# Optimization experiments

Measured on AMD Instinct MI355X. Metric: run time of the kernel, lower is better.

## Reference

```python
import jax, jax.numpy as jnp
import numpy as np

N_NODES = 50000
W_IN = 256
W_OUT = 256
HEADS = 8
D_HEAD = W_OUT // HEADS
NUM_EDGE = 3
N_EDGES = 800000
NEG_SLOPE = 0.2


def setup_inputs() -> dict:
    key = jax.random.key(0)
    ks = jax.random.split(key, 10)
    x = jax.random.normal(ks[0], (N_NODES, W_IN), dtype=jnp.float32)
    adj = jax.random.randint(ks[1], (NUM_EDGE, 2, N_EDGES), 0, N_NODES, dtype=jnp.int64)
    sw = 1.0 / np.sqrt(W_IN)
    # Per-edge-type GATConv params, stacked on leading edge-type axis
    Ws = jax.random.normal(ks[2], (NUM_EDGE, W_IN, HEADS * D_HEAD), dtype=jnp.float32) * sw
    a_l = jax.random.normal(ks[3], (NUM_EDGE, HEADS, D_HEAD), dtype=jnp.float32) * 0.1
    a_r = jax.random.normal(ks[4], (NUM_EDGE, HEADS, D_HEAD), dtype=jnp.float32) * 0.1
    bias = jnp.zeros((NUM_EDGE, HEADS * D_HEAD), dtype=jnp.float32)
    # Semantic attention layer: Linear(w_out -> 1)
    att_w = jax.random.normal(ks[5], (W_OUT, 1), dtype=jnp.float32) * (1.0 / np.sqrt(W_OUT))
    att_b = jnp.zeros((1,), dtype=jnp.float32)
    return {"x": x, "adj": adj, "Ws": Ws, "a_l": a_l, "a_r": a_r,
            "bias": bias, "att_w": att_w, "att_b": att_b}


def _gat(x, edge_index, W, al, ar, b):
    # x: [N, W_IN]; edge_index: [2, E]; W: [W_IN, H*D]; al/ar: [H, D]; b: [H*D]
    N = x.shape[0]
    h = (x @ W).reshape(N, HEADS, D_HEAD)            # [N, H, D]
    src, dst = edge_index[0], edge_index[1]
    el = jnp.einsum('nhd,hd->nh', h, al)             # src-side scores [N, H]
    er = jnp.einsum('nhd,hd->nh', h, ar)             # dst-side scores [N, H]
    e = jax.nn.leaky_relu(el[src] + er[dst], NEG_SLOPE)   # [E, H]
    # segment softmax over incoming edges of each dst node
    m = jax.ops.segment_max(e, dst, num_segments=N)       # [N, H]
    e = jnp.exp(e - m[dst])
    s = jax.ops.segment_sum(e, dst, num_segments=N)       # [N, H]
    alpha = e / (s[dst] + 1e-9)                           # [E, H]
    out = jax.ops.segment_sum(alpha[:, :, None] * h[src], dst, num_segments=N)
    return out.reshape(N, HEADS * D_HEAD) + b             # concat heads [N, W_OUT]


def reference(x, adj, Ws, a_l, a_r, bias, att_w, att_b):
    outs = [_gat(x, adj[i], Ws[i], a_l[i], a_r[i], bias[i]) for i in range(NUM_EDGE)]
    stacked = jnp.stack(outs, axis=1)                     # [N, T, W_OUT]
    # AttentionLayer: scores = Linear(stacked) viewed as [N, 1, T]; NO softmax (faithful)
    att = (stacked @ att_w + att_b).reshape(-1, 1, NUM_EDGE)  # [N, 1, T]
    return jnp.matmul(att, stacked).squeeze(1)            # [N, W_OUT]
```

## Files before the change

kernel.cpp:

```cpp
#include <hip/hip_runtime.h>

#define N_NODES 50000
#define W_IN    256
#define W_OUT   256
#define HEADS   8
#define NUM_T   3
#define N_EDGES 800000
#define NEG_SLOPE 0.2f

#define NB      128
#define BSH     9
#define BNODES  512
#define P1_EPT  16
#define P1_CHUNK (256 * P1_EPT)
#define P1_BLOCKS ((N_EDGES + P1_CHUNK - 1) / P1_CHUNK)
#define NB_USED ((N_NODES + BNODES - 1) / BNODES)

#define GEMM_BLOCKS ((N_NODES + 63) / 64)
#define GATHER_BLOCKS ((N_NODES + 3) / 4)
#define GEMM_SMEM 29696

typedef __attribute__((ext_vector_type(8))) short bf16x8;
typedef __attribute__((ext_vector_type(4))) float f32x4;

__device__ __forceinline__ unsigned short f2b(float f) {
    unsigned u = __float_as_uint(f);
    u = (u + 0x7fffu + ((u >> 16) & 1u)) >> 16;
    return (unsigned short)u;
}
__device__ __forceinline__ float blo(unsigned u) { return __uint_as_float(u << 16); }
__device__ __forceinline__ float bhi(unsigned u) { return __uint_as_float(u & 0xffff0000u); }

__global__ __launch_bounds__(256) void convert_x(const float* __restrict__ x,
                                                 unsigned short* __restrict__ xb) {
    const size_t i = ((size_t)blockIdx.x * 256 + threadIdx.x) * 4;
    const float4 v = *(const float4*)(x + i);
    ushort4 o;
    o.x = f2b(v.x); o.y = f2b(v.y); o.z = f2b(v.z); o.w = f2b(v.w);
    *(ushort4*)(xb + i) = o;
}

__global__ __launch_bounds__(256) void convert_W(const float* __restrict__ Wsrc,
                                                 unsigned short* __restrict__ Wt) {
    const int t = blockIdx.y;
    const int gid = blockIdx.x * 256 + threadIdx.x;
    const int k = gid >> 8, n = gid & 255;
    Wt[(size_t)t * 65536 + (size_t)n * 256 + k] = f2b(Wsrc[(size_t)t * 65536 + gid]);
}

__global__ __launch_bounds__(256) void p1_hist(const int* __restrict__ adj,
                                               int* __restrict__ bucket_cnt) {
    __shared__ int lh[NB];
    const int t = blockIdx.y;
    const int tid = threadIdx.x;
    if (tid < NB) lh[tid] = 0;
    __syncthreads();

    const int* dstp = adj + (size_t)t * 2 * N_EDGES + N_EDGES;
    const int e0 = blockIdx.x * P1_CHUNK + tid * P1_EPT;
#pragma unroll
    for (int i = 0; i < P1_EPT; ++i) {
        const int e = e0 + i;
        if (e < N_EDGES) atomicAdd(&lh[dstp[e] >> BSH], 1);
    }
    __syncthreads();
    if (tid < NB && lh[tid] > 0) atomicAdd(&bucket_cnt[t * NB + tid], lh[tid]);
}

__global__ __launch_bounds__(128) void p1_scan(const int* __restrict__ bucket_cnt,
                                               int* __restrict__ bucket_ptr,
                                               int* __restrict__ bucket_cur) {
    __shared__ int s[NB];
    const int tid = threadIdx.x;
    for (int t = 0; t < NUM_T; ++t) {
        const int v = bucket_cnt[t * NB + tid];
        s[tid] = v;
        __syncthreads();
        for (int off = 1; off < NB; off <<= 1) {
            int o = (tid >= off) ? s[tid - off] : 0;
            __syncthreads();
            s[tid] += o;
            __syncthreads();
        }
        const int incl = s[tid];
        const int excl = incl - v;
        bucket_ptr[t * (NB + 1) + tid] = excl;
        bucket_cur[t * NB + tid] = excl;
        if (tid == NB - 1) bucket_ptr[t * (NB + 1) + NB] = incl;
        __syncthreads();
    }
}

__global__ __launch_bounds__(256) void p1_scatter(const int* __restrict__ adj,
                                                  int* __restrict__ bucket_cur,
                                                  uint2* __restrict__ part) {
    __shared__ int lh[NB];
    __shared__ int loff[NB];
    __shared__ int lbase[NB];
    __shared__ uint2 buf[P1_CHUNK];
    const int t = blockIdx.y;
    const int tid = threadIdx.x;
    const int lane = tid & 63;
    const int wave = tid >> 6;
    if (tid < NB) lh[tid] = 0;
    __syncthreads();

    const int* srcp = adj + (size_t)t * 2 * N_EDGES;
    const int* dstp = srcp + N_EDGES;
    const int e0 = blockIdx.x * P1_CHUNK + tid * P1_EPT;

    int es[P1_EPT], ed[P1_EPT], rk[P1_EPT];
#pragma unroll
    for (int i = 0; i < P1_EPT; ++i) {
        const int e = e0 + i;
        if (e < N_EDGES) {
            es[i] = srcp[e];
            ed[i] = dstp[e];
            rk[i] = atomicAdd(&lh[ed[i] >> BSH], 1);
        } else {
            ed[i] = -1;
        }
    }
    __syncthreads();

    if (tid < NB && lh[tid] > 0)
        lbase[tid] = atomicAdd(&bucket_cur[t * NB + tid], lh[tid]);
    if (wave == 0) {
        const int c0 = lh[lane * 2], c1 = lh[lane * 2 + 1];
        const int s = c0 + c1;
        int run = s;
        for (int off = 1; off < 64; off <<= 1) {
            const int o = __shfl_up(run, off);
            if (lane >= off) run += o;
        }
        const int base = run - s;
        loff[lane * 2] = base;
        loff[lane * 2 + 1] = base + c0;
    }
    __syncthreads();

#pragma unroll
    for (int i = 0; i < P1_EPT; ++i)
        if (ed[i] >= 0)
            buf[loff[ed[i] >> BSH] + rk[i]] =
                make_uint2((unsigned)es[i], (unsigned)ed[i]);
    __syncthreads();

    uint2* pt = part + (size_t)t * N_EDGES;
    int nvalid = N_EDGES - blockIdx.x * P1_CHUNK;
    if (nvalid > P1_CHUNK) nvalid = P1_CHUNK;
    for (int idx = tid; idx < nvalid; idx += 256) {
        const uint2 e = buf[idx];
        const int b = (int)(e.y >> BSH);
        pt[lbase[b] + (idx - loff[b])] = e;
    }
}

__global__ __launch_bounds__(256) void p2_csr(const uint2* __restrict__ part,
                                              const int* __restrict__ bucket_ptr,
                                              int* __restrict__ row_ptr_all,
                                              int* __restrict__ csr_all) {
    __shared__ int sc[BNODES];
    const int b = blockIdx.x;
    const int t = blockIdx.y;
    const int tid = threadIdx.x;
    const int lane = tid & 63;
    const int wave = tid >> 6;

    const uint2* pt = part + (size_t)t * N_EDGES;
    int* row_ptr = row_ptr_all + (size_t)t * (N_NODES + 1);
    int* csr = csr_all + (size_t)t * N_EDGES;

    const int bp0 = bucket_ptr[t * (NB + 1) + b];
    const int bp1 = bucket_ptr[t * (NB + 1) + b + 1];
    const int node0 = b * BNODES;
    int nn = N_NODES - node0; if (nn > BNODES) nn = BNODES;

    sc[tid] = 0; sc[tid + 256] = 0;
    __syncthreads();

    for (int idx = bp0 + tid; idx < bp1; idx += 256)
        atomicAdd(&sc[pt[idx].y - node0], 1);
    __syncthreads();

    if (wave == 0) {
        int v[8], ex[8];
        int s = 0;
#pragma unroll
        for (int i = 0; i < 8; ++i) { v[i] = sc[lane * 8 + i]; ex[i] = s; s += v[i]; }
        int run = s;
        for (int off = 1; off < 64; off <<= 1) {
            int o = __shfl_up(run, off);
            if (lane >= off) run += o;
        }
        const int base = run - s;
#pragma unroll
        for (int i = 0; i < 8; ++i) sc[lane * 8 + i] = base + ex[i];
    }
    __syncthreads();

    for (int i = tid; i < nn; i += 256) row_ptr[node0 + i] = bp0 + sc[i];
    if (b == NB_USED - 1 && tid == 0) row_ptr[N_NODES] = N_EDGES;
    __syncthreads();

    for (int idx = bp0 + tid; idx < bp1; idx += 256) {
        const uint2 e = pt[idx];
        const int pos = bp0 + atomicAdd(&sc[e.y - node0], 1);
        csr[pos] = (int)e.x;
    }
}

__device__ __forceinline__ void gemm_body(const int bm, const int tid,
                                          unsigned char* smem,
                                          const unsigned short* __restrict__ xb,
                                          const unsigned short* __restrict__ Wt,
                                          const float* __restrict__ al,
                                          const float* __restrict__ ar,
                                          unsigned short* __restrict__ H,
                                          float* __restrict__ el,
                                          float* __restrict__ er) {
    unsigned short* As = (unsigned short*)smem;
    unsigned short* Bs = (unsigned short*)(smem + 5120);
    float* els = (float*)(smem + 25600);
    float* ers = (float*)(smem + 27648);

    const int wave = tid >> 6;
    const int lane = tid & 63;
    const int quad = lane >> 4;
    const int l16 = lane & 15;
    const int m0 = bm * 64;

    f32x4 acc[4][4] = {};

    const int arow = tid >> 2;
    const int achunk = (tid & 3) * 8;
    int gm = m0 + arow;
    if (gm > N_NODES - 1) gm = N_NODES - 1;
    const unsigned short* aptr = xb + (size_t)gm * W_IN + achunk;

    for (int k0 = 0; k0 < W_IN; k0 += 32) {
        const uint4 av = *(const uint4*)(aptr + k0);
        *(uint4*)&As[arow * 40 + achunk] = av;
#pragma unroll
        for (int i = 0; i < 4; ++i) {
            const int idx = i * 256 + tid;
            const int brow = idx >> 2;
            const int bch = (idx & 3) * 8;
            const uint4 bv = *(const uint4*)(Wt + (size_t)brow * W_IN + k0 + bch);
            *(uint4*)&Bs[brow * 40 + bch] = bv;
        }
        __syncthreads();

        bf16x8 af[4], bfr[4];
#pragma unroll
        for (int mi = 0; mi < 4; ++mi)
            af[mi] = *(const bf16x8*)&As[(mi * 16 + l16) * 40 + quad * 8];
#pragma unroll
        for (int ni = 0; ni < 4; ++ni)
            bfr[ni] = *(const bf16x8*)&Bs[(wave * 64 + ni * 16 + l16) * 40 + quad * 8];
#pragma unroll
        for (int mi = 0; mi < 4; ++mi)
#pragma unroll
            for (int ni = 0; ni < 4; ++ni)
                acc[mi][ni] = __builtin_amdgcn_mfma_f32_16x16x32_bf16(
                    af[mi], bfr[ni], acc[mi][ni], 0, 0, 0);
        __syncthreads();
    }

#pragma unroll
    for (int mi = 0; mi < 4; ++mi)
#pragma unroll
        for (int reg = 0; reg < 4; ++reg) {
            const int gr = m0 + mi * 16 + quad * 4 + reg;
            if (gr < N_NODES)
#pragma unroll
                for (int ni = 0; ni < 4; ++ni)
                    H[(size_t)gr * W_OUT + wave * 64 + ni * 16 + l16] =
                        f2b(acc[mi][ni][reg]);
        }

    float al4[4], ar4[4];
#pragma unroll
    for (int ni = 0; ni < 4; ++ni) {
        const int c = wave * 64 + ni * 16 + l16;
        al4[ni] = al[c];
        ar4[ni] = ar[c];
    }
#pragma unroll
    for (int mi = 0; mi < 4; ++mi) {
        float pl[4][2] = {}, pr[4][2] = {};
#pragma unroll
        for (int ni = 0; ni < 4; ++ni) {
            const int hl = ni >> 1;
#pragma unroll
            for (int reg = 0; reg < 4; ++reg) {
                pl[reg][hl] += acc[mi][ni][reg] * al4[ni];
                pr[reg][hl] += acc[mi][ni][reg] * ar4[ni];
            }
        }
#pragma unroll
        for (int off = 1; off < 16; off <<= 1)
#pragma unroll
            for (int reg = 0; reg < 4; ++reg)
#pragma unroll
                for (int hl = 0; hl < 2; ++hl) {
                    pl[reg][hl] += __shfl_xor(pl[reg][hl], off);
                    pr[reg][hl] += __shfl_xor(pr[reg][hl], off);
                }
        if (l16 == 0)
#pragma unroll
            for (int reg = 0; reg < 4; ++reg)
#pragma unroll
                for (int hl = 0; hl < 2; ++hl) {
                    const int row = mi * 16 + quad * 4 + reg;
                    els[row * 8 + wave * 2 + hl] = pl[reg][hl];
                    ers[row * 8 + wave * 2 + hl] = pr[reg][hl];
                }
    }
    __syncthreads();

    int nn = N_NODES - m0; if (nn > 64) nn = 64;
    const int nn8 = nn * 8;
    const int i = tid * 4;
    if (i < nn8) {
        *(float4*)(el + (size_t)m0 * 8 + i) = *(float4*)&els[i];
        *(float4*)(er + (size_t)m0 * 8 + i) = *(float4*)&ers[i];
    }
}

__device__ __forceinline__ void gather_body(const int node, const int lane,
                                            const int* __restrict__ csr_src,
                                            const int* __restrict__ row_ptr,
                                            const float* __restrict__ el,
                                            const float* __restrict__ er,
                                            const unsigned short* __restrict__ H,
                                            unsigned short* __restrict__ ot) {
    const int half = lane >> 5;
    const int d8 = lane & 31;
    const int hh = d8 >> 2;

    const int beg = row_ptr[node];
    const int deg = row_ptr[node + 1] - beg;
    const float erv = er[(size_t)node * HEADS + hh];

    float2 acc[4] = {};
    float ssum = 0.f;

    if (deg > 0) {
        int mysrc = (lane < deg) ? csr_src[beg + lane] : 0;
        const int npairs = (deg + 1) >> 1;

        int src0 = __shfl(mysrc, half);
        uint4 u0 = *(const uint4*)(H + (size_t)src0 * W_OUT + d8 * 8);
        float elv0 = el[(size_t)src0 * HEADS + hh];

        for (int q = 0; q < npairs; ++q) {
            int src1 = 0; uint4 u1 = u0; float elv1 = 0.f;
            const int q1 = q + 1;
            if (q1 < npairs) {
                if ((q1 & 31) == 0) {
                    const int cb = beg + (q1 >> 5) * 64;
                    mysrc = (cb + lane < beg + deg) ? csr_src[cb + lane] : 0;
                }
                src1 = __shfl(mysrc, (2 * q1 + half) & 63);
                u1 = *(const uint4*)(H + (size_t)src1 * W_OUT + d8 * 8);
                elv1 = el[(size_t)src1 * HEADS + hh];
            }
            float v = elv0 + erv;
            v = (v > 0.f) ? v : NEG_SLOPE * v;
            const float w = (2 * q + half < deg) ? __expf(v) : 0.f;
            acc[0].x += w * blo(u0.x); acc[0].y += w * bhi(u0.x);
            acc[1].x += w * blo(u0.y); acc[1].y += w * bhi(u0.y);
            acc[2].x += w * blo(u0.z); acc[2].y += w * bhi(u0.z);
            acc[3].x += w * blo(u0.w); acc[3].y += w * bhi(u0.w);
            ssum += w;
            src0 = src1; u0 = u1; elv0 = elv1;
        }
    }

#pragma unroll
    for (int i = 0; i < 4; ++i) {
        acc[i].x += __shfl_xor(acc[i].x, 32);
        acc[i].y += __shfl_xor(acc[i].y, 32);
    }
    ssum += __shfl_xor(ssum, 32);

    if (half == 0) {
        const float inv = 1.f / (ssum + 1e-9f);
        unsigned short o8[8];
#pragma unroll
        for (int i = 0; i < 4; ++i) {
            o8[2 * i]     = f2b(acc[i].x * inv);
            o8[2 * i + 1] = f2b(acc[i].y * inv);
        }
        *(uint4*)(ot + (size_t)node * W_OUT + d8 * 8) = *(const uint4*)o8;
    }
}

__global__ __launch_bounds__(256) void gemm_fused(const unsigned short* __restrict__ xb,
                                                  const unsigned short* __restrict__ Wt,
                                                  const float* __restrict__ al,
                                                  const float* __restrict__ ar,
                                                  unsigned short* __restrict__ H,
                                                  float* __restrict__ el,
                                                  float* __restrict__ er) {
    __shared__ __attribute__((aligned(16))) unsigned char smem[GEMM_SMEM];
    const size_t t = blockIdx.y;
    gemm_body(blockIdx.x, threadIdx.x, smem, xb,
              Wt + t * 65536, al + t * 256, ar + t * 256,
              H + t * (size_t)N_NODES * W_OUT,
              el + t * (size_t)N_NODES * HEADS,
              er + t * (size_t)N_NODES * HEADS);
}

__global__ __launch_bounds__(256) void gat_gather(const int* __restrict__ csr_src,
                                                  const int* __restrict__ row_ptr,
                                                  const float* __restrict__ el,
                                                  const float* __restrict__ er,
                                                  const unsigned short* __restrict__ H,
                                                  unsigned short* __restrict__ ot) {
    const int node = (blockIdx.x * blockDim.x + threadIdx.x) >> 6;
    if (node >= N_NODES) return;
    const size_t t = blockIdx.y;
    gather_body(node, threadIdx.x & 63,
                csr_src + t * N_EDGES, row_ptr + t * (N_NODES + 1),
                el + t * (size_t)N_NODES * HEADS,
                er + t * (size_t)N_NODES * HEADS,
                H + t * (size_t)N_NODES * W_OUT,
                ot + t * (size_t)N_NODES * W_OUT);
}

__global__ __launch_bounds__(256) void combine(const unsigned short* __restrict__ ot,
                                               const float* __restrict__ bias,
                                               const float* __restrict__ att_w,
                                               const float* __restrict__ att_b,
                                               float* __restrict__ out) {
    const int gw = (blockIdx.x * blockDim.x + threadIdx.x) >> 6;
    const int lane = threadIdx.x & 63;
    if (gw >= N_NODES) return;

    const float4 aw = *(const float4*)(att_w + lane * 4);
    const size_t base = (size_t)gw * W_OUT + lane * 4;
    const size_t tstride = (size_t)N_NODES * W_OUT;

    float4 v[NUM_T];
    float p[NUM_T];
#pragma unroll
    for (int t = 0; t < NUM_T; ++t) {
        const uint2 u = *(const uint2*)(ot + t * tstride + base);
        const float4 bv = *(const float4*)(bias + t * W_OUT + lane * 4);
        float4 hv;
        hv.x = blo(u.x) + bv.x;
        hv.y = bhi(u.x) + bv.y;
        hv.z = blo(u.y) + bv.z;
        hv.w = bhi(u.y) + bv.w;
        v[t] = hv;
        p[t] = hv.x * aw.x + hv.y * aw.y + hv.z * aw.z + hv.w * aw.w;
    }
#pragma unroll
    for (int off = 1; off < 64; off <<= 1) {
        p[0] += __shfl_xor(p[0], off);
        p[1] += __shfl_xor(p[1], off);
        p[2] += __shfl_xor(p[2], off);
    }
    const float ab = att_b[0];
    const float a0 = p[0] + ab, a1 = p[1] + ab, a2 = p[2] + ab;
    float4 o;
    o.x = a0 * v[0].x + a1 * v[1].x + a2 * v[2].x;
    o.y = a0 * v[0].y + a1 * v[1].y + a2 * v[2].y;
    o.z = a0 * v[0].z + a1 * v[1].z + a2 * v[2].z;
    o.w = a0 * v[0].w + a1 * v[1].w + a2 * v[2].w;
    *(float4*)(out + base) = o;
}

extern "C" void kernel_launch(void* const* d_in, const int* in_sizes, int n_in,
                              void* d_out, int out_size, void* d_ws, size_t ws_size,
                              hipStream_t stream) {
    const float* x     = (const float*)d_in[0];
    const int*   adj   = (const int*)d_in[1];
    const float* Ws    = (const float*)d_in[2];
    const float* a_l   = (const float*)d_in[3];
    const float* a_r   = (const float*)d_in[4];
    const float* bias  = (const float*)d_in[5];
    const float* att_w = (const float*)d_in[6];
    const float* att_b = (const float*)d_in[7];
    float* out = (float*)d_out;

    const size_t XB_B  = (size_t)N_NODES * W_IN * 2;
    const size_t H_B   = (size_t)N_NODES * W_OUT * 2;
    const size_t WT_B  = (size_t)NUM_T * 65536 * 2;
    const size_t EL_B  = (size_t)N_NODES * HEADS * 4;
    const size_t CSR_B = (size_t)NUM_T * N_EDGES * 4;
    const size_t RP_B  = (size_t)NUM_T * (N_NODES + 1) * 4;
    const size_t MISC_B = (size_t)NUM_T * (NB * 2 + NB + 1) * 4 + 4096;

    const size_t need_merged = XB_B + NUM_T * H_B + WT_B + NUM_T * H_B
                             + 2 * NUM_T * EL_B + CSR_B + RP_B + MISC_B;
    const bool merged = (ws_size >= need_merged);

    char* w = (char*)d_ws;
    unsigned short* xb = (unsigned short*)w; w += XB_B;
    unsigned short* H  = (unsigned short*)w; w += merged ? NUM_T * H_B : H_B;
    unsigned short* Wt = (unsigned short*)w; w += WT_B;
    unsigned short* ot = (unsigned short*)w; w += NUM_T * H_B;
    float* el = (float*)w; w += merged ? NUM_T * EL_B : EL_B;
    float* er = (float*)w; w += merged ? NUM_T * EL_B : EL_B;
    int* csr_src = (int*)w; w += CSR_B;
    int* row_ptr = (int*)w; w += RP_B;
    int* bucket_cnt = (int*)w; w += NUM_T * NB * 4;
    int* bucket_ptr = (int*)w; w += NUM_T * (NB + 1) * 4;
    int* bucket_cur = (int*)w; w += NUM_T * NB * 4;
    uint2* part = (uint2*)ot;

    hipMemsetAsync(bucket_cnt, 0, NUM_T * NB * sizeof(int), stream);
    convert_x<<<12500, 256, 0, stream>>>(x, xb);
    convert_W<<<dim3(256, NUM_T), 256, 0, stream>>>(Ws, Wt);
    p1_hist<<<dim3(P1_BLOCKS, NUM_T), 256, 0, stream>>>(adj, bucket_cnt);
    p1_scan<<<1, 128, 0, stream>>>(bucket_cnt, bucket_ptr, bucket_cur);
    p1_scatter<<<dim3(P1_BLOCKS, NUM_T), 256, 0, stream>>>(adj, bucket_cur, part);
    p2_csr<<<dim3(NB_USED, NUM_T), 256, 0, stream>>>(part, bucket_ptr, row_ptr,
                                                     csr_src);

    if (merged) {
        gemm_fused<<<dim3(GEMM_BLOCKS, NUM_T), 256, 0, stream>>>(
            xb, Wt, a_l, a_r, H, el, er);
        gat_gather<<<dim3(GATHER_BLOCKS, NUM_T), 256, 0, stream>>>(
            csr_src, row_ptr, el, er, H, ot);
    } else {
        for (int t = 0; t < NUM_T; ++t) {
            gemm_fused<<<dim3(GEMM_BLOCKS, 1), 256, 0, stream>>>(
                xb, Wt + (size_t)t * 65536, a_l + t * 256, a_r + t * 256,
                H, el, er);
            gat_gather<<<dim3(GATHER_BLOCKS, 1), 256, 0, stream>>>(
                csr_src + (size_t)t * N_EDGES,
                row_ptr + (size_t)t * (N_NODES + 1),
                el, er, H, ot + (size_t)t * N_NODES * W_OUT);
        }
    }

    combine<<<GATHER_BLOCKS, 256, 0, stream>>>(ot, bias, att_w, att_b, out);
}
```

Baseline: 464.5 us.

## Fuse per-type GAT gather with semantic-attention combine into one kernel

```diff
diff --git a/kernel.cpp b/kernel.cpp
--- a/kernel.cpp
+++ b/kernel.cpp
@@ -328,75 +328,6 @@
     }
 }
 
-__device__ __forceinline__ void gather_body(const int node, const int lane,
-                                            const int* __restrict__ csr_src,
-                                            const int* __restrict__ row_ptr,
-                                            const float* __restrict__ el,
-                                            const float* __restrict__ er,
-                                            const unsigned short* __restrict__ H,
-                                            unsigned short* __restrict__ ot) {
-    const int half = lane >> 5;
-    const int d8 = lane & 31;
-    const int hh = d8 >> 2;
-
-    const int beg = row_ptr[node];
-    const int deg = row_ptr[node + 1] - beg;
-    const float erv = er[(size_t)node * HEADS + hh];
-
-    float2 acc[4] = {};
-    float ssum = 0.f;
-
-    if (deg > 0) {
-        int mysrc = (lane < deg) ? csr_src[beg + lane] : 0;
-        const int npairs = (deg + 1) >> 1;
-
-        int src0 = __shfl(mysrc, half);
-        uint4 u0 = *(const uint4*)(H + (size_t)src0 * W_OUT + d8 * 8);
-        float elv0 = el[(size_t)src0 * HEADS + hh];
-
-        for (int q = 0; q < npairs; ++q) {
-            int src1 = 0; uint4 u1 = u0; float elv1 = 0.f;
-            const int q1 = q + 1;
-            if (q1 < npairs) {
-                if ((q1 & 31) == 0) {
-                    const int cb = beg + (q1 >> 5) * 64;
-                    mysrc = (cb + lane < beg + deg) ? csr_src[cb + lane] : 0;
-                }
-                src1 = __shfl(mysrc, (2 * q1 + half) & 63);
-                u1 = *(const uint4*)(H + (size_t)src1 * W_OUT + d8 * 8);
-                elv1 = el[(size_t)src1 * HEADS + hh];
-            }
-            float v = elv0 + erv;
-            v = (v > 0.f) ? v : NEG_SLOPE * v;
-            const float w = (2 * q + half < deg) ? __expf(v) : 0.f;
-            acc[0].x += w * blo(u0.x); acc[0].y += w * bhi(u0.x);
-            acc[1].x += w * blo(u0.y); acc[1].y += w * bhi(u0.y);
-            acc[2].x += w * blo(u0.z); acc[2].y += w * bhi(u0.z);
-            acc[3].x += w * blo(u0.w); acc[3].y += w * bhi(u0.w);
-            ssum += w;
-            src0 = src1; u0 = u1; elv0 = elv1;
-        }
-    }
-
-#pragma unroll
-    for (int i = 0; i < 4; ++i) {
-        acc[i].x += __shfl_xor(acc[i].x, 32);
-        acc[i].y += __shfl_xor(acc[i].y, 32);
-    }
-    ssum += __shfl_xor(ssum, 32);
-
-    if (half == 0) {
-        const float inv = 1.f / (ssum + 1e-9f);
-        unsigned short o8[8];
-#pragma unroll
-        for (int i = 0; i < 4; ++i) {
-            o8[2 * i]     = f2b(acc[i].x * inv);
-            o8[2 * i + 1] = f2b(acc[i].y * inv);
-        }
-        *(uint4*)(ot + (size_t)node * W_OUT + d8 * 8) = *(const uint4*)o8;
-    }
-}
-
 __global__ __launch_bounds__(256) void gemm_fused(const unsigned short* __restrict__ xb,
                                                   const unsigned short* __restrict__ Wt,
                                                   const float* __restrict__ al,
@@ -413,64 +344,130 @@
               er + t * (size_t)N_NODES * HEADS);
 }
 
-__global__ __launch_bounds__(256) void gat_gather(const int* __restrict__ csr_src,
-                                                  const int* __restrict__ row_ptr,
-                                                  const float* __restrict__ el,
-                                                  const float* __restrict__ er,
-                                                  const unsigned short* __restrict__ H,
-                                                  unsigned short* __restrict__ ot) {
+__device__ __forceinline__ void gather_accum(const int node, const int lane,
+                                             const int* __restrict__ csr_src,
+                                             const int* __restrict__ row_ptr,
+                                             const float* __restrict__ el,
+                                             const float* __restrict__ er,
+                                             const unsigned short* __restrict__ H,
+                                             float2 (&acc)[4], float& ssum) {
+    const int half = lane >> 5;
+    const int d8 = lane & 31;
+    const int hh = d8 >> 2;
+
+    const int beg = row_ptr[node];
+    const int deg = row_ptr[node + 1] - beg;
+    if (deg <= 0) return;
+    const float erv = er[(size_t)node * HEADS + hh];
+
+    int mysrc = (lane < deg) ? csr_src[beg + lane] : 0;
+    const int npairs = (deg + 1) >> 1;
+
+    int src0 = __shfl(mysrc, half);
+    uint4 u0 = *(const uint4*)(H + (size_t)src0 * W_OUT + d8 * 8);
+    float elv0 = el[(size_t)src0 * HEADS + hh];
+
+    for (int q = 0; q < npairs; ++q) {
+        int src1 = 0; uint4 u1 = u0; float elv1 = 0.f;
+        const int q1 = q + 1;
+        if (q1 < npairs) {
+            if ((q1 & 31) == 0) {
+                const int cb = beg + (q1 >> 5) * 64;
+                mysrc = (cb + lane < beg + deg) ? csr_src[cb + lane] : 0;
+            }
+            src1 = __shfl(mysrc, (2 * q1 + half) & 63);
+            u1 = *(const uint4*)(H + (size_t)src1 * W_OUT + d8 * 8);
+            elv1 = el[(size_t)src1 * HEADS + hh];
+        }
+        float v = elv0 + erv;
+        v = (v > 0.f) ? v : NEG_SLOPE * v;
+        const float w = (2 * q + half < deg) ? __expf(v) : 0.f;
+        acc[0].x += w * blo(u0.x); acc[0].y += w * bhi(u0.x);
+        acc[1].x += w * blo(u0.y); acc[1].y += w * bhi(u0.y);
+        acc[2].x += w * blo(u0.z); acc[2].y += w * bhi(u0.z);
+        acc[3].x += w * blo(u0.w); acc[3].y += w * bhi(u0.w);
+        ssum += w;
+        src0 = src1; u0 = u1; elv0 = elv1;
+    }
+}
+
+__global__ __launch_bounds__(256) void gat_gather_all(
+    const int* __restrict__ csr_src, const int* __restrict__ row_ptr,
+    const float* __restrict__ el, const float* __restrict__ er,
+    const unsigned short* __restrict__ H,
+    const float* __restrict__ bias, const float* __restrict__ att_w,
+    const float* __restrict__ att_b, float* __restrict__ out) {
     const int node = (blockIdx.x * blockDim.x + threadIdx.x) >> 6;
+    const int lane = threadIdx.x & 63;
     if (node >= N_NODES) return;
-    const size_t t = blockIdx.y;
-    gather_body(node, threadIdx.x & 63,
-                csr_src + t * N_EDGES, row_ptr + t * (N_NODES + 1),
-                el + t * (size_t)N_NODES * HEADS,
-                er + t * (size_t)N_NODES * HEADS,
-                H + t * (size_t)N_NODES * W_OUT,
-                ot + t * (size_t)N_NODES * W_OUT);
-}
-
-__global__ __launch_bounds__(256) void combine(const unsigned short* __restrict__ ot,
-                                               const float* __restrict__ bias,
-                                               const float* __restrict__ att_w,
-                                               const float* __restrict__ att_b,
-                                               float* __restrict__ out) {
-    const int gw = (blockIdx.x * blockDim.x + threadIdx.x) >> 6;
-    const int lane = threadIdx.x & 63;
-    if (gw >= N_NODES) return;
-
-    const float4 aw = *(const float4*)(att_w + lane * 4);
-    const size_t base = (size_t)gw * W_OUT + lane * 4;
-    const size_t tstride = (size_t)N_NODES * W_OUT;
-
-    float4 v[NUM_T];
-    float p[NUM_T];
+
+    float2 acc[NUM_T][4] = {};
+    float ssum[NUM_T] = {};
+
+#pragma unroll
+    for (int t = 0; t < NUM_T; ++t)
+        gather_accum(node, lane,
+                     csr_src + (size_t)t * N_EDGES,
+                     row_ptr + (size_t)t * (N_NODES + 1),
+                     el + (size_t)t * N_NODES * HEADS,
+                     er + (size_t)t * N_NODES * HEADS,
+                     H + (size_t)t * N_NODES * W_OUT,
+                     acc[t], ssum[t]);
+
 #pragma unroll
     for (int t = 0; t < NUM_T; ++t) {
-        const uint2 u = *(const uint2*)(ot + t * tstride + base);
-        const float4 bv = *(const float4*)(bias + t * W_OUT + lane * 4);
-        float4 hv;
-        hv.x = blo(u.x) + bv.x;
-        hv.y = bhi(u.x) + bv.y;
-        hv.z = blo(u.y) + bv.z;
-        hv.w = bhi(u.y) + bv.w;
-        v[t] = hv;
-        p[t] = hv.x * aw.x + hv.y * aw.y + hv.z * aw.z + hv.w * aw.w;
-    }
-#pragma unroll
-    for (int off = 1; off < 64; off <<= 1) {
-        p[0] += __shfl_xor(p[0], off);
-        p[1] += __shfl_xor(p[1], off);
-        p[2] += __shfl_xor(p[2], off);
-    }
-    const float ab = att_b[0];
-    const float a0 = p[0] + ab, a1 = p[1] + ab, a2 = p[2] + ab;
-    float4 o;
-    o.x = a0 * v[0].x + a1 * v[1].x + a2 * v[2].x;
-    o.y = a0 * v[0].y + a1 * v[1].y + a2 * v[2].y;
-    o.z = a0 * v[0].z + a1 * v[1].z + a2 * v[2].z;
-    o.w = a0 * v[0].w + a1 * v[1].w + a2 * v[2].w;
-    *(float4*)(out + base) = o;
+#pragma unroll
+        for (int i = 0; i < 4; ++i) {
+            acc[t][i].x += __shfl_xor(acc[t][i].x, 32);
+            acc[t][i].y += __shfl_xor(acc[t][i].y, 32);
+        }
+        ssum[t] += __shfl_xor(ssum[t], 32);
+    }
+
+    const int half = lane >> 5;
+    const int d8 = lane & 31;
+    if (half == 0) {
+        const float4 aw0 = *(const float4*)(att_w + d8 * 8);
+        const float4 aw1 = *(const float4*)(att_w + d8 * 8 + 4);
+        float h[NUM_T][8];
+        float p[NUM_T];
+#pragma unroll
+        for (int t = 0; t < NUM_T; ++t) {
+            const float inv = 1.f / (ssum[t] + 1e-9f);
+            const float4 b0 = *(const float4*)(bias + t * W_OUT + d8 * 8);
+            const float4 b1 = *(const float4*)(bias + t * W_OUT + d8 * 8 + 4);
+            h[t][0] = acc[t][0].x * inv + b0.x;
+            h[t][1] = acc[t][0].y * inv + b0.y;
+            h[t][2] = acc[t][1].x * inv + b0.z;
+            h[t][3] = acc[t][1].y * inv + b0.w;
+            h[t][4] = acc[t][2].x * inv + b1.x;
+            h[t][5] = acc[t][2].y * inv + b1.y;
+            h[t][6] = acc[t][3].x * inv + b1.z;
+            h[t][7] = acc[t][3].y * inv + b1.w;
+            p[t] = h[t][0] * aw0.x + h[t][1] * aw0.y + h[t][2] * aw0.z +
+                   h[t][3] * aw0.w + h[t][4] * aw1.x + h[t][5] * aw1.y +
+                   h[t][6] * aw1.z + h[t][7] * aw1.w;
+        }
+#pragma unroll
+        for (int off = 1; off < 32; off <<= 1) {
+            p[0] += __shfl_xor(p[0], off);
+            p[1] += __shfl_xor(p[1], off);
+            p[2] += __shfl_xor(p[2], off);
+        }
+        const float ab = att_b[0];
+        const float a0 = p[0] + ab, a1 = p[1] + ab, a2 = p[2] + ab;
+        float4 o0, o1;
+        o0.x = a0 * h[0][0] + a1 * h[1][0] + a2 * h[2][0];
+        o0.y = a0 * h[0][1] + a1 * h[1][1] + a2 * h[2][1];
+        o0.z = a0 * h[0][2] + a1 * h[1][2] + a2 * h[2][2];
+        o0.w = a0 * h[0][3] + a1 * h[1][3] + a2 * h[2][3];
+        o1.x = a0 * h[0][4] + a1 * h[1][4] + a2 * h[2][4];
+        o1.y = a0 * h[0][5] + a1 * h[1][5] + a2 * h[2][5];
+        o1.z = a0 * h[0][6] + a1 * h[1][6] + a2 * h[2][6];
+        o1.w = a0 * h[0][7] + a1 * h[1][7] + a2 * h[2][7];
+        *(float4*)(out + (size_t)node * W_OUT + d8 * 8) = o0;
+        *(float4*)(out + (size_t)node * W_OUT + d8 * 8 + 4) = o1;
+    }
 }
 
 extern "C" void kernel_launch(void* const* d_in, const int* in_sizes, int n_in,
@@ -486,31 +483,18 @@
     const float* att_b = (const float*)d_in[7];
     float* out = (float*)d_out;
 
-    const size_t XB_B  = (size_t)N_NODES * W_IN * 2;
-    const size_t H_B   = (size_t)N_NODES * W_OUT * 2;
-    const size_t WT_B  = (size_t)NUM_T * 65536 * 2;
-    const size_t EL_B  = (size_t)N_NODES * HEADS * 4;
-    const size_t CSR_B = (size_t)NUM_T * N_EDGES * 4;
-    const size_t RP_B  = (size_t)NUM_T * (N_NODES + 1) * 4;
-    const size_t MISC_B = (size_t)NUM_T * (NB * 2 + NB + 1) * 4 + 4096;
-
-    const size_t need_merged = XB_B + NUM_T * H_B + WT_B + NUM_T * H_B
-                             + 2 * NUM_T * EL_B + CSR_B + RP_B + MISC_B;
-    const bool merged = (ws_size >= need_merged);
-
     char* w = (char*)d_ws;
-    unsigned short* xb = (unsigned short*)w; w += XB_B;
-    unsigned short* H  = (unsigned short*)w; w += merged ? NUM_T * H_B : H_B;
-    unsigned short* Wt = (unsigned short*)w; w += WT_B;
-    unsigned short* ot = (unsigned short*)w; w += NUM_T * H_B;
-    float* el = (float*)w; w += merged ? NUM_T * EL_B : EL_B;
-    float* er = (float*)w; w += merged ? NUM_T * EL_B : EL_B;
-    int* csr_src = (int*)w; w += CSR_B;
-    int* row_ptr = (int*)w; w += RP_B;
+    unsigned short* xb = (unsigned short*)w; w += (size_t)N_NODES * W_IN * 2;
+    unsigned short* H  = (unsigned short*)w; w += (size_t)NUM_T * N_NODES * W_OUT * 2;
+    unsigned short* Wt = (unsigned short*)w; w += (size_t)NUM_T * 65536 * 2;
+    float* el = (float*)w; w += (size_t)NUM_T * N_NODES * HEADS * 4;
+    float* er = (float*)w; w += (size_t)NUM_T * N_NODES * HEADS * 4;
+    int* csr_src = (int*)w; w += (size_t)NUM_T * N_EDGES * 4;
+    int* row_ptr = (int*)w; w += (size_t)NUM_T * (N_NODES + 1) * 4;
     int* bucket_cnt = (int*)w; w += NUM_T * NB * 4;
     int* bucket_ptr = (int*)w; w += NUM_T * (NB + 1) * 4;
     int* bucket_cur = (int*)w; w += NUM_T * NB * 4;
-    uint2* part = (uint2*)ot;
+    uint2* part = (uint2*)H;
 
     hipMemsetAsync(bucket_cnt, 0, NUM_T * NB * sizeof(int), stream);
     convert_x<<<12500, 256, 0, stream>>>(x, xb);
@@ -521,22 +505,9 @@
     p2_csr<<<dim3(NB_USED, NUM_T), 256, 0, stream>>>(part, bucket_ptr, row_ptr,
                                                      csr_src);
 
-    if (merged) {
-        gemm_fused<<<dim3(GEMM_BLOCKS, NUM_T), 256, 0, stream>>>(
-            xb, Wt, a_l, a_r, H, el, er);
-        gat_gather<<<dim3(GATHER_BLOCKS, NUM_T), 256, 0, stream>>>(
-            csr_src, row_ptr, el, er, H, ot);
-    } else {
-        for (int t = 0; t < NUM_T; ++t) {
-            gemm_fused<<<dim3(GEMM_BLOCKS, 1), 256, 0, stream>>>(
-                xb, Wt + (size_t)t * 65536, a_l + t * 256, a_r + t * 256,
-                H, el, er);
-            gat_gather<<<dim3(GATHER_BLOCKS, 1), 256, 0, stream>>>(
-                csr_src + (size_t)t * N_EDGES,
-                row_ptr + (size_t)t * (N_NODES + 1),
-                el, er, H, ot + (size_t)t * N_NODES * W_OUT);
-        }
-    }
-
-    combine<<<GATHER_BLOCKS, 256, 0, stream>>>(ot, bias, att_w, att_b, out);
-}
+    gemm_fused<<<dim3(GEMM_BLOCKS, NUM_T), 256, 0, stream>>>(
+        xb, Wt, a_l, a_r, H, el, er);
+
+    gat_gather_all<<<GATHER_BLOCKS, 256, 0, stream>>>(
+        csr_src, row_ptr, el, er, H, bias, att_w, att_b, out);
+}
```

Result: no change. 467.2 us (+0.6%).
